# Kernel tuning notes

Measured on AMD Instinct MI355X. Metric: run time of the kernel, lower is better.

## Reference

```python
import jax, jax.numpy as jnp
import numpy as np

EMBED = 1024
B, T = 4, 2048

def setup_inputs() -> dict:
    key = jax.random.key(0)
    k1, k2, k3, k4, k5 = jax.random.split(key, 5)
    s_in = 1.0 / np.sqrt(EMBED)
    return {
        "x": jax.random.normal(k1, (B, T, EMBED), dtype=jnp.float32),
        "w_qkv": jax.random.normal(k2, (3 * EMBED, EMBED), dtype=jnp.float32) * s_in,  # torch Linear layout [out,in]
        "b_qkv": jax.random.normal(k3, (3 * EMBED,), dtype=jnp.float32) * 0.01,
        "w_proj": jax.random.normal(k4, (EMBED, EMBED), dtype=jnp.float32) * s_in,
        "b_proj": jax.random.normal(k5, (EMBED,), dtype=jnp.float32) * 0.01,
    }

def reference(x, w_qkv, b_qkv, w_proj, b_proj):
    Bq, Tq, C = x.shape
    qkv = jnp.einsum('btc,oc->bto', x, w_qkv) + b_qkv        # [B,T,3C]
    q, k, v = jnp.split(qkv, 3, axis=-1)                      # each [B,T,C]
    att = jnp.einsum('btc,bsc->bts', q, k) / jnp.sqrt(jnp.float32(C))  # [B,T,T]
    causal = jnp.tril(jnp.ones((Tq, Tq), dtype=bool))
    att = jnp.where(causal[None, :, :], att, -jnp.inf)
    att = jax.nn.softmax(att, axis=-1)
    out = jnp.einsum('bts,bsc->btc', att, v)                   # [B,T,C]
    return jnp.einsum('btc,oc->bto', out, w_proj) + b_proj
```

## Files before the change

kernel.cpp:

```cpp
#include <hip/hip_runtime.h>
#include <hip/hip_bf16.h>

typedef __hip_bfloat16 bf16;
typedef __attribute__((ext_vector_type(8))) short bf16x8;
typedef __attribute__((ext_vector_type(4))) float f32x4;

#define GLD16(gp, lp) __builtin_amdgcn_global_load_lds( \
    (const __attribute__((address_space(1))) void*)(gp), \
    (__attribute__((address_space(3))) void*)(lp), 16, 0, 0)

__global__ __launch_bounds__(256) void cvt_bf16(const float* __restrict__ in,
                                                bf16* __restrict__ out) {
    int i = (blockIdx.x * 256 + threadIdx.x) * 4;
    float4 f = *(const float4*)&in[i];
    __hip_bfloat162 p0, p1;
    p0.x = __float2bfloat16(f.x); p0.y = __float2bfloat16(f.y);
    p1.x = __float2bfloat16(f.z); p1.y = __float2bfloat16(f.w);
    *(__hip_bfloat162*)&out[i]     = p0;
    *(__hip_bfloat162*)&out[i + 2] = p1;
}

__global__ __launch_bounds__(256) void cvt_weights(
    const float* __restrict__ wq, bf16* __restrict__ wqo,
    const float* __restrict__ wp, bf16* __restrict__ wpo) {
    int blk = blockIdx.x;
    const float* in; bf16* out; int base;
    if (blk < 3072) { in = wq; out = wqo; base = blk; }
    else            { in = wp; out = wpo; base = blk - 3072; }
    int i = (base * 256 + threadIdx.x) * 4;
    float4 f = *(const float4*)&in[i];
    __hip_bfloat162 p0, p1;
    p0.x = __float2bfloat16(f.x); p0.y = __float2bfloat16(f.y);
    p1.x = __float2bfloat16(f.z); p1.y = __float2bfloat16(f.w);
    *(__hip_bfloat162*)&out[i]     = p0;
    *(__hip_bfloat162*)&out[i + 2] = p1;
}

__global__ void transpose_v(const bf16* __restrict__ V, bf16* __restrict__ Vt) {
    __shared__ bf16 tile[32][33];
    const int b = blockIdx.z;
    const int c0 = blockIdx.x * 32, t0 = blockIdx.y * 32;
    const int tx = threadIdx.x, ty = threadIdx.y;
    #pragma unroll
    for (int i = 0; i < 32; i += 8)
        tile[ty + i][tx] = V[((size_t)(b * 2048 + t0 + ty + i)) * 1024 + c0 + tx];
    __syncthreads();
    #pragma unroll
    for (int i = 0; i < 32; i += 8)
        Vt[((size_t)b * 1024 + c0 + ty + i) * 2048 + t0 + tx] = tile[tx][ty + i];
}

__global__ __launch_bounds__(256) void softmax_causal(float* __restrict__ S) {
    const int row = blockIdx.x;
    const int t = row & 2047;
    float* srow = S + (size_t)row * 2048;
    bf16* prow = (bf16*)srow;
    const int tid = threadIdx.x;
    const int base = tid * 8;
    float4 f0 = *(const float4*)&srow[base];
    float4 f1 = *(const float4*)&srow[base + 4];
    float v[8] = {f0.x, f0.y, f0.z, f0.w, f1.x, f1.y, f1.z, f1.w};
    float lmax = -INFINITY;
    #pragma unroll
    for (int i = 0; i < 8; ++i) {
        v[i] = (base + i <= t) ? v[i] : -INFINITY;
        lmax = fmaxf(lmax, v[i]);
    }
    #pragma unroll
    for (int off = 32; off; off >>= 1) lmax = fmaxf(lmax, __shfl_xor(lmax, off));
    __shared__ float red[4];
    const int wave = tid >> 6, lane = tid & 63;
    if (lane == 0) red[wave] = lmax;
    __syncthreads();
    lmax = fmaxf(fmaxf(red[0], red[1]), fmaxf(red[2], red[3]));
    float lsum = 0.f;
    #pragma unroll
    for (int i = 0; i < 8; ++i) { v[i] = __expf(v[i] - lmax); lsum += v[i]; }
    #pragma unroll
    for (int off = 32; off; off >>= 1) lsum += __shfl_xor(lsum, off);
    __syncthreads();
    if (lane == 0) red[wave] = lsum;
    __syncthreads();
    lsum = red[0] + red[1] + red[2] + red[3];
    const float inv = 1.f / lsum;
    #pragma unroll
    for (int i = 0; i < 8; ++i) prow[base + i] = __float2bfloat16(v[i] * inv);
}

template<int MODE>
__global__ __launch_bounds__(512, 2) void gemm256(
    const bf16* __restrict__ A, const bf16* __restrict__ B,
    const float* __restrict__ bias,
    void* __restrict__ out0, void* __restrict__ out1, void* __restrict__ out2)
{
    __shared__ bf16 As[2][256][64];
    __shared__ bf16 Bs[2][256][64];
    constexpr int LDA = (MODE == 2) ? 4096 : 1024;
    constexpr int LDB = (MODE == 2) ? 2048 : 1024;

    const int bx = blockIdx.x, by = blockIdx.y, bz = blockIdx.z;
    if (MODE == 1 && bx > by) return;
    const int NT = (MODE == 2) ? 4 * (by + 1) : 16;
    const int m0 = by * 256, n0 = bx * 256;

    const bf16* Ab = A;
    const bf16* Bb = B;
    if (MODE == 1) { Ab += (size_t)bz * (2048ull * 1024); Bb += (size_t)bz * (2048ull * 1024); }
    if (MODE == 2) { Ab += (size_t)bz * (2048ull * 4096); Bb += (size_t)bz * (1024ull * 2048); }

    const int tid = threadIdx.x;
    const int lane = tid & 63, wave = tid >> 6;
    const int wr = wave >> 2, wc = wave & 3;
    const int frow = lane & 15, fk = lane >> 4, fx = lane & 7;

    const int rl = tid >> 3;
    const int scol = ((tid & 7) ^ (rl & 7)) * 8;
    const bf16* pAsrc = Ab + (size_t)(m0 + rl) * LDA + scol;
    const bf16* pBsrc = Bb + (size_t)(n0 + rl) * LDB + scol;
    const int dchunk = tid * 8;

    f32x4 acc[4][4][2] = {};

    #define STG(P, LD, LDSBASE, H, K0) do { \
        GLD16((P) + (size_t)(H) * 128 * (LD) + (K0), (LDSBASE) + (H) * 8192 + dchunk); \
        GLD16((P) + (size_t)((H) * 128 + 64) * (LD) + (K0), (LDSBASE) + (H) * 8192 + 4096 + dchunk); \
    } while (0)

    {
        bf16* la = &As[0][0][0]; bf16* lb = &Bs[0][0][0];
        STG(pAsrc, LDA, la, 0, 0);
        STG(pBsrc, LDB, lb, 0, 0);
        STG(pBsrc, LDB, lb, 1, 0);
        STG(pAsrc, LDA, la, 1, 0);
        asm volatile("s_waitcnt vmcnt(4)" ::: "memory");
        __builtin_amdgcn_s_barrier();
    }

    for (int t = 0; t < NT; ++t) {
        const int buf = t & 1, nbuf = buf ^ 1;
        const int kn = (t + 1) * 64;
        bf16* lan = &As[nbuf][0][0]; bf16* lbn = &Bs[nbuf][0][0];
        const bool more = (t + 1 < NT);

        #pragma unroll
        for (int q = 0; q < 4; ++q) {
            const int aR = ((q >> 1) << 7) + wr * 64 + frow;
            const int bR = ((q & 1) << 7) + wc * 32 + frow;
            bf16x8 av[4][2], bv[2][2];
            #pragma unroll
            for (int m = 0; m < 4; ++m)
                #pragma unroll
                for (int ks = 0; ks < 2; ++ks)
                    av[m][ks] = *(const bf16x8*)
                        &As[buf][aR + m * 16][((((ks << 2) | fk) ^ fx) << 3)];
            #pragma unroll
            for (int n = 0; n < 2; ++n)
                #pragma unroll
                for (int ks = 0; ks < 2; ++ks)
                    bv[n][ks] = *(const bf16x8*)
                        &Bs[buf][bR + n * 16][((((ks << 2) | fk) ^ fx) << 3)];

            if (more) {
                if (q == 0)      STG(pAsrc, LDA, lan, 0, kn);
                else if (q == 1) STG(pBsrc, LDB, lbn, 0, kn);
                else if (q == 2) STG(pBsrc, LDB, lbn, 1, kn);
                else             STG(pAsrc, LDA, lan, 1, kn);
            }

            __builtin_amdgcn_sched_barrier(0);
            __builtin_amdgcn_s_barrier();
            asm volatile("s_waitcnt lgkmcnt(0)" ::: "memory");
            __builtin_amdgcn_sched_barrier(0);

            __builtin_amdgcn_s_setprio(1);
            #pragma unroll
            for (int m = 0; m < 4; ++m)
                #pragma unroll
                for (int n = 0; n < 2; ++n)
                    #pragma unroll
                    for (int ks = 0; ks < 2; ++ks)
                        acc[q][m][n] = __builtin_amdgcn_mfma_f32_16x16x32_bf16(
                            av[m][ks], bv[n][ks], acc[q][m][n], 0, 0, 0);
            __builtin_amdgcn_s_setprio(0);
            __builtin_amdgcn_sched_barrier(0);

            if (more) {
                if (q != 2) asm volatile("s_waitcnt vmcnt(4)" ::: "memory");
            } else {
                if (q == 0)      asm volatile("s_waitcnt vmcnt(2)" ::: "memory");
                else if (q == 1) asm volatile("s_waitcnt vmcnt(0)" ::: "memory");
            }
            __builtin_amdgcn_s_barrier();
        }
    }
    #undef STG

    #pragma unroll
    for (int q = 0; q < 4; ++q) {
        #pragma unroll
        for (int m = 0; m < 4; ++m) {
            #pragma unroll
            for (int n = 0; n < 2; ++n) {
                #pragma unroll
                for (int j = 0; j < 4; ++j) {
                    const int gr = m0 + ((q >> 1) << 7) + wr * 64 + m * 16 + (fk << 2) + j;
                    const int gc = n0 + ((q & 1) << 7) + wc * 32 + n * 16 + frow;
                    float v = acc[q][m][n][j];
                    if (MODE == 0) {
                        v += bias[gc];
                        const int which = gc >> 10;
                        const int col = gc & 1023;
                        bf16* dst = which == 0 ? (bf16*)out0
                                  : which == 1 ? (bf16*)out1 : (bf16*)out2;
                        dst[(size_t)gr * 1024 + col] = __float2bfloat16(v);
                    } else if (MODE == 1) {
                        ((float*)out0)[(size_t)bz * (2048ull * 2048) +
                                       (size_t)gr * 2048 + gc] = v * 0.03125f;
                    } else if (MODE == 2) {
                        ((bf16*)out0)[((size_t)bz * 2048 + gr) * 1024 + gc] =
                            __float2bfloat16(v);
                    } else {
                        ((float*)out0)[(size_t)gr * 1024 + gc] = v + bias[gc];
                    }
                }
            }
        }
    }
}

extern "C" void kernel_launch(void* const* d_in, const int* in_sizes, int n_in,
                              void* d_out, int out_size, void* d_ws, size_t ws_size,
                              hipStream_t stream) {
    const float* x      = (const float*)d_in[0];
    const float* w_qkv  = (const float*)d_in[1];
    const float* b_qkv  = (const float*)d_in[2];
    const float* w_proj = (const float*)d_in[3];
    const float* b_proj = (const float*)d_in[4];
    float* out = (float*)d_out;
    char* ws = (char*)d_ws;

    bf16* Xb = (bf16*)(ws);
    bf16* Wq = (bf16*)(ws + 16777216);
    bf16* Wp = (bf16*)(ws + 23068672);
    bf16* Qb = (bf16*)(ws + 25165824);
    bf16* Kb = (bf16*)(ws + 41943040);
    bf16* Vb = (bf16*)(ws + 58720256);
    float* S = (float*)(ws + 75497472);
    bf16* Vt = Xb;
    bf16* O  = Qb;

    hipLaunchKernelGGL(cvt_bf16, dim3(8192), dim3(256), 0, stream, x, Xb);
    hipLaunchKernelGGL(cvt_weights, dim3(4096), dim3(256), 0, stream,
                       w_qkv, Wq, w_proj, Wp);

    gemm256<0><<<dim3(12, 32, 1), 512, 0, stream>>>(
        Xb, Wq, b_qkv, (void*)Qb, (void*)Kb, (void*)Vb);

    hipLaunchKernelGGL(transpose_v, dim3(32, 64, 4), dim3(32, 8), 0, stream, Vb, Vt);

    gemm256<1><<<dim3(8, 8, 4), 512, 0, stream>>>(
        Qb, Kb, (const float*)nullptr, (void*)S, nullptr, nullptr);

    hipLaunchKernelGGL(softmax_causal, dim3(8192), dim3(256), 0, stream, S);

    gemm256<2><<<dim3(4, 8, 4), 512, 0, stream>>>(
        (const bf16*)S, Vt, (const float*)nullptr, (void*)O, nullptr, nullptr);

    gemm256<3><<<dim3(4, 32, 1), 512, 0, stream>>>(
        O, Wp, b_proj, (void*)out, nullptr, nullptr);
}
```

Baseline: 364.9 us.

## Fuse exp into QK GEMM epilogue, defer softmax normalization to PV GEMM

The QK^T GEMM epilogue now applies the scale, exponentiates without max-subtraction, applies the causal mask and writes bf16 P instead of fp32 scores. A small row-sum kernel replaces the full softmax pass, and the PV GEMM divides by the row sum in its epilogue. This cuts the fp32 score write plus the read-modify-write softmax pass, halving the attention matrix traffic. It also adds an XCD-aware workgroup index remap to every GEMM. The lack of max-subtraction risks overflow for large logits, and the row sum is taken from bf16-rounded values.

```diff
diff --git a/kernel.cpp b/kernel.cpp
--- a/kernel.cpp
+++ b/kernel.cpp
@@ -50,41 +50,27 @@
         Vt[((size_t)b * 1024 + c0 + ty + i) * 2048 + t0 + tx] = tile[tx][ty + i];
 }
 
-__global__ __launch_bounds__(256) void softmax_causal(float* __restrict__ S) {
+__global__ __launch_bounds__(256) void rowsum_p(const bf16* __restrict__ P,
+                                                float* __restrict__ rs) {
     const int row = blockIdx.x;
     const int t = row & 2047;
-    float* srow = S + (size_t)row * 2048;
-    bf16* prow = (bf16*)srow;
+    const int ncol = ((t >> 8) + 1) << 8;
+    const bf16* prow = P + (size_t)row * 2048;
     const int tid = threadIdx.x;
-    const int base = tid * 8;
-    float4 f0 = *(const float4*)&srow[base];
-    float4 f1 = *(const float4*)&srow[base + 4];
-    float v[8] = {f0.x, f0.y, f0.z, f0.w, f1.x, f1.y, f1.z, f1.w};
-    float lmax = -INFINITY;
-    #pragma unroll
-    for (int i = 0; i < 8; ++i) {
-        v[i] = (base + i <= t) ? v[i] : -INFINITY;
-        lmax = fmaxf(lmax, v[i]);
-    }
-    #pragma unroll
-    for (int off = 32; off; off >>= 1) lmax = fmaxf(lmax, __shfl_xor(lmax, off));
+    float s = 0.f;
+    if (tid * 8 < ncol) {
+        bf16x8 v = *(const bf16x8*)&prow[tid * 8];
+        #pragma unroll
+        for (int i = 0; i < 8; ++i)
+            s += __bfloat162float(((const bf16*)&v)[i]);
+    }
+    #pragma unroll
+    for (int off = 32; off; off >>= 1) s += __shfl_xor(s, off);
     __shared__ float red[4];
     const int wave = tid >> 6, lane = tid & 63;
-    if (lane == 0) red[wave] = lmax;
+    if (lane == 0) red[wave] = s;
     __syncthreads();
-    lmax = fmaxf(fmaxf(red[0], red[1]), fmaxf(red[2], red[3]));
-    float lsum = 0.f;
-    #pragma unroll
-    for (int i = 0; i < 8; ++i) { v[i] = __expf(v[i] - lmax); lsum += v[i]; }
-    #pragma unroll
-    for (int off = 32; off; off >>= 1) lsum += __shfl_xor(lsum, off);
-    __syncthreads();
-    if (lane == 0) red[wave] = lsum;
-    __syncthreads();
-    lsum = red[0] + red[1] + red[2] + red[3];
-    const float inv = 1.f / lsum;
-    #pragma unroll
-    for (int i = 0; i < 8; ++i) prow[base + i] = __float2bfloat16(v[i] * inv);
+    if (tid == 0) rs[row] = red[0] + red[1] + red[2] + red[3];
 }
 
 template<int MODE>
@@ -95,10 +81,15 @@
 {
     __shared__ bf16 As[2][256][64];
     __shared__ bf16 Bs[2][256][64];
-    constexpr int LDA = (MODE == 2) ? 4096 : 1024;
+    constexpr int LDA = (MODE == 2) ? 2048 : 1024;
     constexpr int LDB = (MODE == 2) ? 2048 : 1024;
 
-    const int bx = blockIdx.x, by = blockIdx.y, bz = blockIdx.z;
+    const int nwgx = gridDim.x;
+    const int nwg = nwgx * gridDim.y;
+    int wg = blockIdx.y * nwgx + blockIdx.x;
+    wg = (wg & 7) * (nwg >> 3) + (wg >> 3);
+    const int bx = wg % nwgx, by = wg / nwgx, bz = blockIdx.z;
+
     if (MODE == 1 && bx > by) return;
     const int NT = (MODE == 2) ? 4 * (by + 1) : 16;
     const int m0 = by * 256, n0 = bx * 256;
@@ -106,7 +97,7 @@
     const bf16* Ab = A;
     const bf16* Bb = B;
     if (MODE == 1) { Ab += (size_t)bz * (2048ull * 1024); Bb += (size_t)bz * (2048ull * 1024); }
-    if (MODE == 2) { Ab += (size_t)bz * (2048ull * 4096); Bb += (size_t)bz * (1024ull * 2048); }
+    if (MODE == 2) { Ab += (size_t)bz * (2048ull * 2048); Bb += (size_t)bz * (1024ull * 2048); }
 
     const int tid = threadIdx.x;
     const int lane = tid & 63, wave = tid >> 6;
@@ -214,11 +205,14 @@
                                   : which == 1 ? (bf16*)out1 : (bf16*)out2;
                         dst[(size_t)gr * 1024 + col] = __float2bfloat16(v);
                     } else if (MODE == 1) {
-                        ((float*)out0)[(size_t)bz * (2048ull * 2048) +
-                                       (size_t)gr * 2048 + gc] = v * 0.03125f;
+                        float p = __expf(v * 0.03125f);
+                        if (gc > gr) p = 0.f;
+                        ((bf16*)out0)[(size_t)bz * (2048ull * 2048) +
+                                      (size_t)gr * 2048 + gc] = __float2bfloat16(p);
                     } else if (MODE == 2) {
+                        const float inv = 1.f / bias[bz * 2048 + gr];
                         ((bf16*)out0)[((size_t)bz * 2048 + gr) * 1024 + gc] =
-                            __float2bfloat16(v);
+                            __float2bfloat16(v * inv);
                     } else {
                         ((float*)out0)[(size_t)gr * 1024 + gc] = v + bias[gc];
                     }
@@ -245,7 +239,8 @@
     bf16* Qb = (bf16*)(ws + 25165824);
     bf16* Kb = (bf16*)(ws + 41943040);
     bf16* Vb = (bf16*)(ws + 58720256);
-    float* S = (float*)(ws + 75497472);
+    bf16* P  = (bf16*)(ws + 75497472);
+    float* RS = (float*)(ws + 75497472 + 33554432);
     bf16* Vt = Xb;
     bf16* O  = Qb;
 
@@ -259,12 +254,12 @@
     hipLaunchKernelGGL(transpose_v, dim3(32, 64, 4), dim3(32, 8), 0, stream, Vb, Vt);
 
     gemm256<1><<<dim3(8, 8, 4), 512, 0, stream>>>(
-        Qb, Kb, (const float*)nullptr, (void*)S, nullptr, nullptr);
-
-    hipLaunchKernelGGL(softmax_causal, dim3(8192), dim3(256), 0, stream, S);
+        Qb, Kb, (const float*)nullptr, (void*)P, nullptr, nullptr);
+
+    hipLaunchKernelGGL(rowsum_p, dim3(8192), dim3(256), 0, stream, P, RS);
 
     gemm256<2><<<dim3(4, 8, 4), 512, 0, stream>>>(
-        (const bf16*)S, Vt, (const float*)nullptr, (void*)O, nullptr, nullptr);
+        P, Vt, (const float*)RS, (void*)O, nullptr, nullptr);
 
     gemm256<3><<<dim3(4, 32, 1), 512, 0, stream>>>(
         O, Wp, b_proj, (void*)out, nullptr, nullptr);
```

New measurement: 357.8 us. Within noise of the previous version (-1.9%).
